# Optimization experiments

Measured on AMD Instinct MI355X. Metric: run time of the kernel, lower is better.

The kernel has to match this reference:

```python
import jax, jax.numpy as jnp
import numpy as np

NUM_NODES = 100000
NUM_HYPEREDGES = 100000
NNZ = 1600000
K = 64
LAMBDA_ORTHO = 0.1


def setup_inputs() -> dict:
    key = jax.random.key(0)
    k1, k2, k3 = jax.random.split(key, 3)
    Z = jax.random.normal(k1, (NUM_NODES, K), dtype=jnp.float32)
    hyperedge_index = jax.random.randint(k2, (2, NNZ), 0, NUM_HYPEREDGES, dtype=jnp.int64)
    hyperedge_weight = jax.random.uniform(k3, (NUM_HYPEREDGES,), dtype=jnp.float32)
    return {
        "Z": Z,
        "hyperedge_index": hyperedge_index,
        "num_nodes": NUM_NODES,
        "hyperedge_weight": hyperedge_weight,
    }


def reference(Z, hyperedge_index, num_nodes, hyperedge_weight):
    E = hyperedge_weight.shape[0]  # num_hyperedges (static)
    node_idx = hyperedge_index[0]
    edge_idx = hyperedge_index[1]

    # Node degree Dv = sum of incident hyperedge weights; clamp zeros to 1.
    w_exp = hyperedge_weight[edge_idx]                                  # [nnz]
    Dv = jax.ops.segment_sum(w_exp, node_idx, num_segments=num_nodes)   # [N]
    Dv = jnp.where(Dv == 0, jnp.ones_like(Dv), Dv)
    Y = Z * (Dv ** -0.5)[:, None]                                       # [N, k]

    # Hyperedge cardinality De (clamped) and raw counts n_e.
    ones = jnp.ones_like(edge_idx, dtype=Z.dtype)
    n_e = jax.ops.segment_sum(ones, edge_idx, num_segments=E)           # [E]
    De = jnp.where(n_e == 0, jnp.ones_like(n_e), n_e)

    # Closed form for the per-edge pairwise-distance loop:
    # 0.5 * sum_{i,j in e} |y_i - y_j|^2 = n_e * sum_i |y_i|^2 - |sum_i y_i|^2
    Yg = Y[node_idx]                                                    # [nnz, k]
    sum_e = jax.ops.segment_sum(Yg, edge_idx, num_segments=E)           # [E, k]
    ss_e = jax.ops.segment_sum(jnp.sum(Yg * Yg, axis=-1), edge_idx, num_segments=E)  # [E]
    per_edge = n_e * ss_e - jnp.sum(sum_e * sum_e, axis=-1)             # [E]
    loss = jnp.sum(hyperedge_weight / De * per_edge)

    # Orthogonality penalty: ||Y^T Y - I||_F
    k = Z.shape[1]
    G = Y.T @ Y - jnp.eye(k, dtype=Z.dtype)
    ortho_loss = jnp.sqrt(jnp.sum(G * G))

    return loss + LAMBDA_ORTHO * ortho_loss
```

## Files before the change

### kernel.cpp

```cpp
#include <hip/hip_runtime.h>
#include <math.h>

#define NNODES 100000
#define NEDGES 100000
#define NNZV   1600000
#define KDIM   64
#define LAMBDA 0.1f

#define NB    782
#define BSH   7
#define BMASK 127
#define CAP   3072
#define A0B   256
#define A0T   1024
#define CHUNK 6250
#define GMB   256
#define DUMMYN 100000u

#define OFF_G       0
#define OFF_PART    16384
#define OFF_ZN      19712
#define OFF_GC1     23040
#define OFF_GC2     26368
#define OFF_S1      29696
#define OFF_S2      9638912
#define OFF_YQ      19248128

typedef float f32x2 __attribute__((ext_vector_type(2)));

#if defined(__has_builtin)
#if __has_builtin(__builtin_amdgcn_cvt_f32_fp8)
#define HAS_CVT_FP8 1
#endif
#if __has_builtin(__builtin_amdgcn_cvt_pk_fp8_f32)
#define HAS_PK_FP8 1
#endif
#if __has_builtin(__builtin_amdgcn_cvt_pk_f32_fp8)
#define HAS_PK_F32_FP8 1
#endif
#endif

__device__ __forceinline__ int load_node(const unsigned* idx, int i, bool i64) {
    return (int)(i64 ? idx[2 * i] : idx[i]);
}
__device__ __forceinline__ int load_edge(const unsigned* idx, int i, bool i64) {
    return (int)(i64 ? idx[2 * (NNZV + i)] : idx[NNZV + i]);
}

__device__ __forceinline__ unsigned char enc_fp8(float x) {
    unsigned u = __float_as_uint(x);
    unsigned s = (u >> 31) << 7;
    unsigned mag = u & 0x7FFFFFFFu;
    if (mag >= 0x43E00000u) return (unsigned char)(s | 0x7Eu);
    if (mag < 0x3C800000u) {
        float a = __uint_as_float(mag);
        int m = (int)rintf(a * 512.0f);
        if (m >= 8) return (unsigned char)(s | 0x08u);
        return (unsigned char)(s | (unsigned)m);
    }
    unsigned lsb = (mag >> 20) & 1u;
    mag += 0x0007FFFFu + lsb;
    unsigned e = (mag >> 23) - 120u;
    return (unsigned char)(s | (e << 3) | ((mag >> 20) & 7u));
}

__device__ __forceinline__ unsigned pack_fp8x4(float y0, float y1, float y2, float y3) {
#ifdef HAS_PK_FP8
    int q = 0;
    q = __builtin_amdgcn_cvt_pk_fp8_f32(y0, y1, q, false);
    q = __builtin_amdgcn_cvt_pk_fp8_f32(y2, y3, q, true);
    return (unsigned)q;
#else
    return (unsigned)enc_fp8(y0) | ((unsigned)enc_fp8(y1) << 8) |
           ((unsigned)enc_fp8(y2) << 16) | ((unsigned)enc_fp8(y3) << 24);
#endif
}

template <int SEL>
__device__ __forceinline__ float dec_fp8(unsigned v) {
#ifdef HAS_CVT_FP8
    return __builtin_amdgcn_cvt_f32_fp8(v, SEL);
#else
    unsigned b = (v >> (8 * SEL)) & 0xFFu;
    unsigned e = (b >> 3) & 15u, m = b & 7u;
    float f = e ? __uint_as_float(((e + 120u) << 23) | (m << 20))
                : (float)m * 0.001953125f;
    return (b & 128u) ? -f : f;
#endif
}

__device__ __forceinline__ void dec4_fp8(unsigned v, float& a0, float& a1,
                                         float& a2, float& a3) {
#ifdef HAS_PK_F32_FP8
    f32x2 lo = __builtin_amdgcn_cvt_pk_f32_fp8((int)v, false);
    f32x2 hi = __builtin_amdgcn_cvt_pk_f32_fp8((int)v, true);
    a0 = lo.x; a1 = lo.y; a2 = hi.x; a3 = hi.y;
#else
    a0 = dec_fp8<0>(v); a1 = dec_fp8<1>(v);
    a2 = dec_fp8<2>(v); a3 = dec_fp8<3>(v);
#endif
}

__global__ void init_kernel(unsigned* __restrict__ gcur1,
                            unsigned* __restrict__ gcur2,
                            float* __restrict__ G,
                            unsigned* __restrict__ Yq32) {
    int i = blockIdx.x * 256 + threadIdx.x;
    if (i < NB) {
        gcur1[i] = (unsigned)i * CAP;
        gcur2[i] = (unsigned)i * CAP;
    }
    if (i < KDIM * KDIM) G[i] = 0.0f;
    if (i < 16) Yq32[DUMMYN * 16u + i] = 0u;
}

__global__ __launch_bounds__(A0T) void sort_kernel(const unsigned* __restrict__ idx,
                                                   unsigned* __restrict__ gcur1,
                                                   unsigned* __restrict__ gcur2,
                                                   unsigned* __restrict__ S1,
                                                   unsigned* __restrict__ S2) {
    __shared__ unsigned stage[CHUNK];
    __shared__ unsigned lhist[NB], lcur[NB], gbase[NB];
    __shared__ unsigned wsum[16], fred[16];
    int which = blockIdx.x >> 8, chunk = blockIdx.x & (A0B - 1);
    int t = threadIdx.x, wave = t >> 6, lane = t & 63;

    unsigned hv = idx[2 * t + 1];
#pragma unroll
    for (int off = 32; off; off >>= 1) hv |= __shfl_xor(hv, off);
    if (lane == 0) fred[wave] = hv;
    for (int j = t; j < NB; j += A0T) lhist[j] = 0u;
    __syncthreads();
    unsigned o = 0;
#pragma unroll
    for (int k = 0; k < 16; ++k) o |= fred[k];
    bool i64 = (o == 0u);

    int base = chunk * CHUNK;
    unsigned nd[7], ed[7];
#pragma unroll
    for (int k = 0; k < 7; ++k) {
        bool ok = (k < 6) || (t < CHUNK - 6 * A0T);
        int i = base + k * A0T + t;
        nd[k] = ok ? (unsigned)load_node(idx, i, i64) : 0u;
        ed[k] = ok ? (unsigned)load_edge(idx, i, i64) : 0u;
    }

#pragma unroll
    for (int k = 0; k < 7; ++k) {
        bool ok = (k < 6) || (t < CHUNK - 6 * A0T);
        if (ok) atomicAdd(&lhist[(which ? nd[k] : ed[k]) >> BSH], 1u);
    }
    __syncthreads();

    unsigned v = (t < NB) ? lhist[t] : 0u;
    unsigned x = v;
#pragma unroll
    for (int off = 1; off < 64; off <<= 1) {
        unsigned y = __shfl_up(x, off);
        if (lane >= off) x += y;
    }
    if (lane == 63) wsum[wave] = x;
    __syncthreads();
    if (t < 16) {
        unsigned a = wsum[t], y = a;
#pragma unroll
        for (int off = 1; off < 16; off <<= 1) {
            unsigned z = __shfl_up(y, off);
            if (t >= off) y += z;
        }
        wsum[t] = y - a;
    }
    __syncthreads();
    if (t < NB) lcur[t] = wsum[wave] + x - v;
    __syncthreads();

#pragma unroll
    for (int k = 0; k < 7; ++k) {
        bool ok = (k < 6) || (t < CHUNK - 6 * A0T);
        if (ok) {
            unsigned key, val;
            if (which == 0) {
                key = ed[k] >> BSH;
                val = nd[k] | ((ed[k] & BMASK) << 17);
            } else {
                key = nd[k] >> BSH;
                val = ed[k] | ((nd[k] & BMASK) << 17);
            }
            unsigned p = atomicAdd(&lcur[key], 1u);
            stage[p] = val;
        }
    }
    __syncthreads();

    unsigned* gcur = which ? gcur2 : gcur1;
    if (t < NB) {
        unsigned c = lhist[t];
        gbase[t] = c ? atomicAdd(&gcur[t], c) : 0u;
    }
    __syncthreads();

    unsigned* S = which ? S2 : S1;
    int li = lane & 7;
    for (int bb = wave * 8 + (lane >> 3); bb < NB; bb += 128) {
        unsigned c = lhist[bb];
        unsigned st = lcur[bb] - c;
        unsigned g = gbase[bb];
        for (unsigned m = li; m < c; m += 8) S[g + m] = stage[st + m];
    }
}

__global__ __launch_bounds__(256) void dvyq_kernel(const unsigned* __restrict__ S2,
                                                   const unsigned* __restrict__ gcur2,
                                                   const float* __restrict__ w,
                                                   const float* __restrict__ Z,
                                                   unsigned* __restrict__ Yq32,
                                                   float* __restrict__ ZN) {
    __shared__ float accd[128];
    __shared__ float red[256];
    int t = threadIdx.x, b = blockIdx.x;
    if (t < 128) accd[t] = 0.0f;
    __syncthreads();
    unsigned cnt = gcur2[b] - (unsigned)b * CAP;
    const unsigned* src = S2 + (size_t)b * CAP;
    for (unsigned i = t; i < cnt; i += 256) {
        unsigned e = src[i];
        atomicAdd(&accd[e >> 17], w[e & 0x1FFFFu]);
    }
    __syncthreads();
    int base = b * 128;
    float zn = 0.0f;
    for (int j = t; j < 128 * 16; j += 256) {
        int row = j >> 4, q = j & 15;
        int node = base + row;
        if (node < NNODES) {
            float4 v = ((const float4*)Z)[node * 16 + q];
            float d = accd[row];
            bool good = d > 0.0f;
            float r = good ? rsqrtf(d) : 1.0f;
            zn += good ? (v.x * v.x + v.y * v.y + v.z * v.z + v.w * v.w) : 0.0f;
            Yq32[node * 16 + q] = pack_fp8x4(v.x * r, v.y * r, v.z * r, v.w * r);
        }
    }
    red[t] = zn;
    __syncthreads();
    for (int s = 128; s > 0; s >>= 1) {
        if (t < s) red[t] += red[t + s];
        __syncthreads();
    }
    if (t == 0) ZN[b] = red[0];
}

__global__ __launch_bounds__(512) void bg_kernel(const unsigned* __restrict__ Yq32,
                                                 const float* __restrict__ w,
                                                 const unsigned* __restrict__ S1,
                                                 const unsigned* __restrict__ gcur1,
                                                 float* __restrict__ part,
                                                 float* __restrict__ G) {
    __shared__ unsigned lhist[128], loffs[128], lcur[128];
    __shared__ unsigned snode[CAP];
    __shared__ float wred[8];
    __shared__ float ys[64][KDIM];
    int t = threadIdx.x, b = blockIdx.x;

    if (b >= NB) {
        int gb = b - NB;
        float acc[8];
#pragma unroll
        for (int i = 0; i < 8; ++i) acc[i] = 0.0f;
        int c = t & 63;
        int r0 = ((t >> 6) & 7) * 8;
        for (int base = gb * 64; base < NNODES; base += GMB * 64) {
            int rows = min(64, NNODES - base);
            __syncthreads();
            for (int j = t; j < rows * 16; j += 512) {
                unsigned v = Yq32[base * 16 + j];
                int row = j >> 4, q4 = (j & 15) * 4;
                float x0, x1, x2, x3;
                dec4_fp8(v, x0, x1, x2, x3);
                ys[row][q4 + 0] = x0;
                ys[row][q4 + 1] = x1;
                ys[row][q4 + 2] = x2;
                ys[row][q4 + 3] = x3;
            }
            __syncthreads();
#pragma unroll 4
            for (int i = 0; i < rows; ++i) {
                float yc = ys[i][c];
#pragma unroll
                for (int rr = 0; rr < 8; ++rr) acc[rr] += ys[i][r0 + rr] * yc;
            }
        }
#pragma unroll
        for (int rr = 0; rr < 8; ++rr) atomicAdd(&G[(r0 + rr) * KDIM + c], acc[rr]);
        return;
    }

    if (t < 128) lhist[t] = 0u;
    __syncthreads();
    unsigned cnt = gcur1[b] - (unsigned)b * CAP;
    const unsigned* src = S1 + (size_t)b * CAP;
    for (unsigned i = t; i < cnt; i += 512)
        atomicAdd(&lhist[src[i] >> 17], 1u);
    __syncthreads();
    if (t < 64) {
        unsigned a = lhist[2 * t], bb = lhist[2 * t + 1];
        unsigned sp = a + bb, x = sp;
#pragma unroll
        for (int off = 1; off < 64; off <<= 1) {
            unsigned y = __shfl_up(x, off);
            if (t >= off) x += y;
        }
        unsigned ex = x - sp;
        loffs[2 * t] = ex;          lcur[2 * t] = ex;
        loffs[2 * t + 1] = ex + a;  lcur[2 * t + 1] = ex + a;
    }
    __syncthreads();
    for (unsigned i = t; i < cnt; i += 512) {
        unsigned e = src[i];
        unsigned pos = atomicAdd(&lcur[e >> 17], 1u);
        snode[pos] = e & 0x1FFFFu;
    }
    __syncthreads();
    int wv = t >> 6, lane = t & 63, ms = lane >> 4, kq = lane & 15;
    float acc = 0.0f;
    for (int el = wv; el < 64; el += 8) {
        int eA = el, eB = el + 64;
        unsigned nA = lhist[eA], nB = lhist[eB];
        if (nA == 0 && nB == 0) continue;
        unsigned begA = loffs[eA], begB = loffs[eB];
        float a0 = 0, a1 = 0, a2 = 0, a3 = 0;
        float c0 = 0, c1 = 0, c2 = 0, c3 = 0;
        unsigned mmax = nA > nB ? nA : nB;
        for (unsigned m = 0; m < mmax; m += 16) {
            unsigned mA0 = m + (unsigned)ms, mA1 = mA0 + 4, mA2 = mA0 + 8, mA3 = mA0 + 12;
            unsigned nA0 = (mA0 < nA) ? snode[begA + mA0] : DUMMYN;
            unsigned nA1 = (mA1 < nA) ? snode[begA + mA1] : DUMMYN;
            unsigned nA2 = (mA2 < nA) ? snode[begA + mA2] : DUMMYN;
            unsigned nA3 = (mA3 < nA) ? snode[begA + mA3] : DUMMYN;
            unsigned nB0 = (mA0 < nB) ? snode[begB + mA0] : DUMMYN;
            unsigned nB1 = (mA1 < nB) ? snode[begB + mA1] : DUMMYN;
            unsigned nB2 = (mA2 < nB) ? snode[begB + mA2] : DUMMYN;
            unsigned nB3 = (mA3 < nB) ? snode[begB + mA3] : DUMMYN;
            unsigned vA0 = Yq32[nA0 * 16u + (unsigned)kq];
            unsigned vA1 = Yq32[nA1 * 16u + (unsigned)kq];
            unsigned vA2 = Yq32[nA2 * 16u + (unsigned)kq];
            unsigned vA3 = Yq32[nA3 * 16u + (unsigned)kq];
            unsigned vB0 = Yq32[nB0 * 16u + (unsigned)kq];
            unsigned vB1 = Yq32[nB1 * 16u + (unsigned)kq];
            unsigned vB2 = Yq32[nB2 * 16u + (unsigned)kq];
            unsigned vB3 = Yq32[nB3 * 16u + (unsigned)kq];
            float x0, x1, x2, x3;
            dec4_fp8(vA0, x0, x1, x2, x3);
            a0 += x0; a1 += x1; a2 += x2; a3 += x3;
            dec4_fp8(vA1, x0, x1, x2, x3);
            a0 += x0; a1 += x1; a2 += x2; a3 += x3;
            dec4_fp8(vA2, x0, x1, x2, x3);
            a0 += x0; a1 += x1; a2 += x2; a3 += x3;
            dec4_fp8(vA3, x0, x1, x2, x3);
            a0 += x0; a1 += x1; a2 += x2; a3 += x3;
            dec4_fp8(vB0, x0, x1, x2, x3);
            c0 += x0; c1 += x1; c2 += x2; c3 += x3;
            dec4_fp8(vB1, x0, x1, x2, x3);
            c0 += x0; c1 += x1; c2 += x2; c3 += x3;
            dec4_fp8(vB2, x0, x1, x2, x3);
            c0 += x0; c1 += x1; c2 += x2; c3 += x3;
            dec4_fp8(vB3, x0, x1, x2, x3);
            c0 += x0; c1 += x1; c2 += x2; c3 += x3;
        }
        a0 += __shfl_xor(a0, 16); a0 += __shfl_xor(a0, 32);
        a1 += __shfl_xor(a1, 16); a1 += __shfl_xor(a1, 32);
        a2 += __shfl_xor(a2, 16); a2 += __shfl_xor(a2, 32);
        a3 += __shfl_xor(a3, 16); a3 += __shfl_xor(a3, 32);
        c0 += __shfl_xor(c0, 16); c0 += __shfl_xor(c0, 32);
        c1 += __shfl_xor(c1, 16); c1 += __shfl_xor(c1, 32);
        c2 += __shfl_xor(c2, 16); c2 += __shfl_xor(c2, 32);
        c3 += __shfl_xor(c3, 16); c3 += __shfl_xor(c3, 32);
        float aa = a0 * a0 + a1 * a1 + a2 * a2 + a3 * a3;
        float cc = c0 * c0 + c1 * c1 + c2 * c2 + c3 * c3;
        aa += __shfl_xor(aa, 1); aa += __shfl_xor(aa, 2);
        aa += __shfl_xor(aa, 4); aa += __shfl_xor(aa, 8);
        cc += __shfl_xor(cc, 1); cc += __shfl_xor(cc, 2);
        cc += __shfl_xor(cc, 4); cc += __shfl_xor(cc, 8);
        if (lane == 0) {
            if (nA) acc += (w[b * 128 + eA] / (float)nA) * aa;
            if (nB) acc += (w[b * 128 + eB] / (float)nB) * cc;
        }
    }
    if (lane == 0) wred[wv] = acc;
    __syncthreads();
    if (t == 0) {
        float s = 0.0f;
        for (int i = 0; i < 8; ++i) s += wred[i];
        part[b] = s;
    }
}

__global__ void final_kernel(const float* __restrict__ G,
                             const float* __restrict__ ZN,
                             const float* __restrict__ part,
                             float* __restrict__ out) {
    __shared__ float r1[256], r2[256];
    int t = threadIdx.x;
    float zn = 0.0f, pe = 0.0f, gg = 0.0f;
    for (int i = t; i < NB; i += 256) { zn += ZN[i]; pe += part[i]; }
    for (int i = t; i < KDIM * KDIM; i += 256) {
        int r = i >> 6, c = i & 63;
        float g = G[i] - ((r == c) ? 1.0f : 0.0f);
        gg += g * g;
    }
    r1[t] = zn - pe; r2[t] = gg;
    __syncthreads();
    for (int s = 128; s > 0; s >>= 1) {
        if (t < s) { r1[t] += r1[t + s]; r2[t] += r2[t + s]; }
        __syncthreads();
    }
    if (t == 0) out[0] = r1[0] + LAMBDA * sqrtf(r2[0]);
}

extern "C" void kernel_launch(void* const* d_in, const int* in_sizes, int n_in,
                              void* d_out, int out_size, void* d_ws, size_t ws_size,
                              hipStream_t stream) {
    const float* Z = (const float*)d_in[0];
    const unsigned* idx = (const unsigned*)d_in[1];
    const float* w = (const float*)d_in[3];
    float* out = (float*)d_out;
    char* ws = (char*)d_ws;

    float* G        = (float*)(ws + OFF_G);
    float* part     = (float*)(ws + OFF_PART);
    float* ZN       = (float*)(ws + OFF_ZN);
    unsigned* gcur1 = (unsigned*)(ws + OFF_GC1);
    unsigned* gcur2 = (unsigned*)(ws + OFF_GC2);
    unsigned* S1    = (unsigned*)(ws + OFF_S1);
    unsigned* S2    = (unsigned*)(ws + OFF_S2);
    unsigned* Yq32  = (unsigned*)(ws + OFF_YQ);

    init_kernel<<<16, 256, 0, stream>>>(gcur1, gcur2, G, Yq32);
    sort_kernel<<<2 * A0B, A0T, 0, stream>>>(idx, gcur1, gcur2, S1, S2);
    dvyq_kernel<<<NB, 256, 0, stream>>>(S2, gcur2, w, Z, Yq32, ZN);
    bg_kernel<<<NB + GMB, 512, 0, stream>>>(Yq32, w, S1, gcur1, part, G);
    final_kernel<<<1, 256, 0, stream>>>(G, ZN, part, out);
}
```

Baseline: 106.2 us.

## Fuse both bucket sorts into one pass reading indices once

The sort kernel used to launch separate block groups for edge-keyed and node-keyed bucketing, so each group read the whole index array. Now each of 512 blocks loads a smaller chunk once and runs both bucketings in sequence, halving global index reads. The scatter uses 4 lanes per bucket instead of 8, and the Gram block count in bg_kernel changes from 256 to 242. This costs an extra serialized pass per block, more synchronisation, and smaller per-bucket runs when writing out to global memory.

```diff
diff --git a/kernel.cpp b/kernel.cpp
--- a/kernel.cpp
+++ b/kernel.cpp
@@ -11,10 +11,10 @@
 #define BSH   7
 #define BMASK 127
 #define CAP   3072
-#define A0B   256
-#define A0T   1024
-#define CHUNK 6250
-#define GMB   256
+#define SB    512
+#define ST    1024
+#define CH2   3125
+#define GMB   242
 #define DUMMYN 100000u
 
 #define OFF_G       0
@@ -114,99 +114,102 @@
     if (i < 16) Yq32[DUMMYN * 16u + i] = 0u;
 }
 
-__global__ __launch_bounds__(A0T) void sort_kernel(const unsigned* __restrict__ idx,
-                                                   unsigned* __restrict__ gcur1,
-                                                   unsigned* __restrict__ gcur2,
-                                                   unsigned* __restrict__ S1,
-                                                   unsigned* __restrict__ S2) {
-    __shared__ unsigned stage[CHUNK];
+__global__ __launch_bounds__(ST) void sort_kernel(const unsigned* __restrict__ idx,
+                                                  unsigned* __restrict__ gcur1,
+                                                  unsigned* __restrict__ gcur2,
+                                                  unsigned* __restrict__ S1,
+                                                  unsigned* __restrict__ S2) {
+    __shared__ unsigned stage[CH2];
     __shared__ unsigned lhist[NB], lcur[NB], gbase[NB];
     __shared__ unsigned wsum[16], fred[16];
-    int which = blockIdx.x >> 8, chunk = blockIdx.x & (A0B - 1);
     int t = threadIdx.x, wave = t >> 6, lane = t & 63;
+    int base = blockIdx.x * CH2;
 
     unsigned hv = idx[2 * t + 1];
 #pragma unroll
     for (int off = 32; off; off >>= 1) hv |= __shfl_xor(hv, off);
     if (lane == 0) fred[wave] = hv;
-    for (int j = t; j < NB; j += A0T) lhist[j] = 0u;
+    for (int j = t; j < NB; j += ST) lhist[j] = 0u;
     __syncthreads();
     unsigned o = 0;
 #pragma unroll
     for (int k = 0; k < 16; ++k) o |= fred[k];
     bool i64 = (o == 0u);
 
-    int base = chunk * CHUNK;
-    unsigned nd[7], ed[7];
-#pragma unroll
-    for (int k = 0; k < 7; ++k) {
-        bool ok = (k < 6) || (t < CHUNK - 6 * A0T);
-        int i = base + k * A0T + t;
+    unsigned nd[4], ed[4];
+#pragma unroll
+    for (int k = 0; k < 4; ++k) {
+        bool ok = (k < 3) || (t < CH2 - 3 * ST);
+        int i = base + k * ST + t;
         nd[k] = ok ? (unsigned)load_node(idx, i, i64) : 0u;
         ed[k] = ok ? (unsigned)load_edge(idx, i, i64) : 0u;
     }
 
 #pragma unroll
-    for (int k = 0; k < 7; ++k) {
-        bool ok = (k < 6) || (t < CHUNK - 6 * A0T);
-        if (ok) atomicAdd(&lhist[(which ? nd[k] : ed[k]) >> BSH], 1u);
-    }
-    __syncthreads();
-
-    unsigned v = (t < NB) ? lhist[t] : 0u;
-    unsigned x = v;
-#pragma unroll
-    for (int off = 1; off < 64; off <<= 1) {
-        unsigned y = __shfl_up(x, off);
-        if (lane >= off) x += y;
-    }
-    if (lane == 63) wsum[wave] = x;
-    __syncthreads();
-    if (t < 16) {
-        unsigned a = wsum[t], y = a;
-#pragma unroll
-        for (int off = 1; off < 16; off <<= 1) {
-            unsigned z = __shfl_up(y, off);
-            if (t >= off) y += z;
-        }
-        wsum[t] = y - a;
-    }
-    __syncthreads();
-    if (t < NB) lcur[t] = wsum[wave] + x - v;
-    __syncthreads();
-
-#pragma unroll
-    for (int k = 0; k < 7; ++k) {
-        bool ok = (k < 6) || (t < CHUNK - 6 * A0T);
-        if (ok) {
-            unsigned key, val;
-            if (which == 0) {
-                key = ed[k] >> BSH;
-                val = nd[k] | ((ed[k] & BMASK) << 17);
-            } else {
-                key = nd[k] >> BSH;
-                val = ed[k] | ((nd[k] & BMASK) << 17);
+    for (int which = 0; which < 2; ++which) {
+#pragma unroll
+        for (int k = 0; k < 4; ++k) {
+            bool ok = (k < 3) || (t < CH2 - 3 * ST);
+            if (ok) atomicAdd(&lhist[(which ? nd[k] : ed[k]) >> BSH], 1u);
+        }
+        __syncthreads();
+        unsigned v = (t < NB) ? lhist[t] : 0u;
+        unsigned x = v;
+#pragma unroll
+        for (int off = 1; off < 64; off <<= 1) {
+            unsigned y = __shfl_up(x, off);
+            if (lane >= off) x += y;
+        }
+        if (lane == 63) wsum[wave] = x;
+        __syncthreads();
+        if (t < 16) {
+            unsigned a = wsum[t], y = a;
+#pragma unroll
+            for (int off = 1; off < 16; off <<= 1) {
+                unsigned z = __shfl_up(y, off);
+                if (t >= off) y += z;
             }
-            unsigned p = atomicAdd(&lcur[key], 1u);
-            stage[p] = val;
-        }
-    }
-    __syncthreads();
-
-    unsigned* gcur = which ? gcur2 : gcur1;
-    if (t < NB) {
-        unsigned c = lhist[t];
-        gbase[t] = c ? atomicAdd(&gcur[t], c) : 0u;
-    }
-    __syncthreads();
-
-    unsigned* S = which ? S2 : S1;
-    int li = lane & 7;
-    for (int bb = wave * 8 + (lane >> 3); bb < NB; bb += 128) {
-        unsigned c = lhist[bb];
-        unsigned st = lcur[bb] - c;
-        unsigned g = gbase[bb];
-        for (unsigned m = li; m < c; m += 8) S[g + m] = stage[st + m];
+            wsum[t] = y - a;
+        }
+        __syncthreads();
+        if (t < NB) lcur[t] = wsum[wave] + x - v;
+        __syncthreads();
+#pragma unroll
+        for (int k = 0; k < 4; ++k) {
+            bool ok = (k < 3) || (t < CH2 - 3 * ST);
+            if (ok) {
+                unsigned key, val;
+                if (which == 0) {
+                    key = ed[k] >> BSH;
+                    val = nd[k] | ((ed[k] & BMASK) << 17);
+                } else {
+                    key = nd[k] >> BSH;
+                    val = ed[k] | ((nd[k] & BMASK) << 17);
+                }
+                unsigned p = atomicAdd(&lcur[key], 1u);
+                stage[p] = val;
+            }
+        }
+        __syncthreads();
+        unsigned* gcur = which ? gcur2 : gcur1;
+        if (t < NB) {
+            unsigned c = lhist[t];
+            gbase[t] = c ? atomicAdd(&gcur[t], c) : 0u;
+        }
+        __syncthreads();
+        unsigned* S = which ? S2 : S1;
+        int li = lane & 3;
+        for (int bb = wave * 16 + (lane >> 2); bb < NB; bb += 256) {
+            unsigned c = lhist[bb];
+            unsigned st = lcur[bb] - c;
+            unsigned g = gbase[bb];
+            for (unsigned m = li; m < c; m += 4) S[g + m] = stage[st + m];
+        }
+        if (which == 0) {
+            __syncthreads();
+            for (int j = t; j < NB; j += ST) lhist[j] = 0u;
+            __syncthreads();
+        }
     }
 }
 
@@ -437,7 +440,7 @@
     unsigned* Yq32  = (unsigned*)(ws + OFF_YQ);
 
     init_kernel<<<16, 256, 0, stream>>>(gcur1, gcur2, G, Yq32);
-    sort_kernel<<<2 * A0B, A0T, 0, stream>>>(idx, gcur1, gcur2, S1, S2);
+    sort_kernel<<<SB, ST, 0, stream>>>(idx, gcur1, gcur2, S1, S2);
     dvyq_kernel<<<NB, 256, 0, stream>>>(S2, gcur2, w, Z, Yq32, ZN);
     bg_kernel<<<NB + GMB, 512, 0, stream>>>(Yq32, w, S1, gcur1, part, G);
     final_kernel<<<1, 256, 0, stream>>>(G, ZN, part, out);
```

Result: no change. 104.3 us (median of 2 runs) (-1.8%).
